# Optimization experiments

Measured on AMD Instinct MI355X. Metric: run time of the kernel, lower is better.

The kernel has to match this reference:

```python
import jax, jax.numpy as jnp
import numpy as np

N, K, D, L = 4096, 64, 1024, 16384  # tokens, top-k, d_in, num_latents


def setup_inputs() -> dict:
    key = jax.random.key(0)
    ks = jax.random.split(key, 9)
    x = jax.random.normal(ks[0], (N, D), jnp.float32)
    y = jax.random.normal(ks[1], (N, D), jnp.float32)
    latent_acts = jax.random.uniform(ks[2], (N, K), jnp.float32)  # post-topk acts (nonneg)
    latent_indices = jax.random.randint(ks[3], (N, K), 0, L)
    W_dec = jax.random.normal(ks[4], (L, D), jnp.float32) / np.sqrt(D).astype(np.float32)
    b_dec = jax.random.normal(ks[5], (D,), jnp.float32) * 0.01
    post_enc = jax.random.normal(ks[6], (L,), jnp.float32) * 0.01
    post_enc_scale = 1.0 + 0.1 * jax.random.normal(ks[7], (L,), jnp.float32)
    W_skip = jax.random.normal(ks[8], (D, D), jnp.float32) / np.sqrt(D).astype(np.float32)
    return {
        "x": x, "y": y,
        "latent_acts": latent_acts, "latent_indices": latent_indices,
        "W_dec": W_dec, "b_dec": b_dec,
        "post_enc": post_enc, "post_enc_scale": post_enc_scale,
        "W_skip": W_skip,
    }


def reference(x, y, latent_acts, latent_indices, W_dec, b_dec, post_enc, post_enc_scale, W_skip):
    # current_latent_acts: per-index bias gather + indexed scaling
    acts = (latent_acts + post_enc[latent_indices]) * post_enc_scale[latent_indices]  # [N,K]
    # decode: gather W_dec rows by top-k indices, weighted combine, add decoder bias
    sae_out = jnp.einsum('nk,nkd->nd', acts, W_dec[latent_indices]) + b_dec  # [N,D]
    # skip connection: x @ W_skip.mT
    sae_out = sae_out + x @ W_skip.T
    # FVU loss
    e = y - sae_out
    total_variance = jnp.sum((y - jnp.mean(y, axis=0)) ** 2)
    fvu = jnp.sum(e ** 2) / total_variance
    return sae_out, fvu
```

## Files before the change

### kernel.cpp

```cpp
#include <hip/hip_runtime.h>
#include <hip/hip_bf16.h>
#include <cstdint>

#define N_TOK 4096
#define KTOP  64
#define DIM   1024
#define NLAT  16384
#define NCHUNK 8

typedef __bf16 bf16x8 __attribute__((ext_vector_type(8)));
typedef float  floatx4 __attribute__((ext_vector_type(4)));
typedef float  floatx2 __attribute__((ext_vector_type(2)));

#define GLOBAL_AS(p) ((const __attribute__((address_space(1))) void*)(p))
#define LDS_AS(p)    ((__attribute__((address_space(3))) void*)(p))

__device__ inline unsigned short f2bf(float f){
  unsigned int u = __float_as_uint(f);
  unsigned int r = (u + 0x7fffu + ((u >> 16) & 1u)) >> 16;
  return (unsigned short)r;
}

__global__ __launch_bounds__(256) void prep(
    const float* __restrict__ x, const float* __restrict__ Wsk,
    const float* __restrict__ Wd, const float* __restrict__ y,
    unsigned short* __restrict__ xb, unsigned short* __restrict__ wb,
    unsigned char* __restrict__ wdf,
    float* __restrict__ colsum, float* __restrict__ sumsq){
  const int b = blockIdx.x;
  const int t = threadIdx.x;
  if (b < 1024){
    int i0 = b * 1024 + t;
    #pragma unroll
    for (int i = 0; i < 4; i++){
      float4 v = ((const float4*)x)[i0 + i * 256];
      ushort4 o; o.x = f2bf(v.x); o.y = f2bf(v.y); o.z = f2bf(v.z); o.w = f2bf(v.w);
      ((ushort4*)xb)[i0 + i * 256] = o;
    }
  } else if (b < 1280){
    int i0 = (b - 1024) * 1024 + t;
    #pragma unroll
    for (int i = 0; i < 4; i++){
      float4 v = ((const float4*)Wsk)[i0 + i * 256];
      ushort4 o; o.x = f2bf(v.x); o.y = f2bf(v.y); o.z = f2bf(v.z); o.w = f2bf(v.w);
      ((ushort4*)wb)[i0 + i * 256] = o;
    }
  } else if (b < 3328){
    int lat0 = (b - 1280) * 8;
    const int chunk = t >> 5;
    const int off   = (t & 31) * 4;
    #pragma unroll
    for (int r = 0; r < 8; r++){
      int lat = lat0 + r;
      float4 v = ((const float4*)(Wd + (size_t)lat * DIM))[t];
      int p = __builtin_amdgcn_cvt_pk_fp8_f32(v.x, v.y, 0, false);
      p     = __builtin_amdgcn_cvt_pk_fp8_f32(v.z, v.w, p, true);
      *(int*)(wdf + ((size_t)chunk * NLAT + lat) * 128 + off) = p;
    }
  } else {
    const int r0 = (b - 3328) * 8;
    float4 cs = {0.f, 0.f, 0.f, 0.f};
    float sq = 0.f;
    #pragma unroll
    for (int r = 0; r < 8; r++){
      float4 v = ((const float4*)(y + (size_t)(r0 + r) * DIM))[t];
      cs.x += v.x; cs.y += v.y; cs.z += v.z; cs.w += v.w;
      sq += v.x*v.x + v.y*v.y + v.z*v.z + v.w*v.w;
    }
    atomicAdd(&colsum[t*4+0], cs.x);
    atomicAdd(&colsum[t*4+1], cs.y);
    atomicAdd(&colsum[t*4+2], cs.z);
    atomicAdd(&colsum[t*4+3], cs.w);
    #pragma unroll
    for (int off = 32; off > 0; off >>= 1) sq += __shfl_down(sq, off, 64);
    __shared__ float s_red[4];
    if ((t & 63) == 0) s_red[t >> 6] = sq;
    __syncthreads();
    if (t == 0) atomicAdd(sumsq, s_red[0] + s_red[1] + s_red[2] + s_red[3]);
  }
}

__global__ __launch_bounds__(256) void skip_gemm(
    const unsigned short* __restrict__ xb,
    const unsigned short* __restrict__ wb,
    const float* __restrict__ b_dec,
    float* __restrict__ out){
  __shared__ unsigned short As[128][32];
  __shared__ unsigned short Bs[64][32];
  const int row0 = blockIdx.x * 128;
  const int col0 = blockIdx.y * 64;
  const int t    = threadIdx.x;
  const int lane = t & 63;
  const int w    = t >> 6;
  const int wr   = w * 32;
  const int lm   = lane & 15;
  const int kq   = lane >> 4;
  const int sr   = t >> 2;
  const int sc   = (t & 3) * 8;

  floatx4 acc[2][4] = {};

  for (int k0 = 0; k0 < DIM; k0 += 32){
    __builtin_amdgcn_global_load_lds(GLOBAL_AS(xb + (size_t)(row0 + sr) * DIM + k0 + sc),
                                     LDS_AS(&As[sr][sc]), 16, 0, 0);
    __builtin_amdgcn_global_load_lds(GLOBAL_AS(xb + (size_t)(row0 + 64 + sr) * DIM + k0 + sc),
                                     LDS_AS(&As[64 + sr][sc]), 16, 0, 0);
    __builtin_amdgcn_global_load_lds(GLOBAL_AS(wb + (size_t)(col0 + sr) * DIM + k0 + sc),
                                     LDS_AS(&Bs[sr][sc]), 16, 0, 0);
    __syncthreads();
    bf16x8 af[2], bfr[4];
    #pragma unroll
    for (int mi = 0; mi < 2; mi++) af[mi] = *(const bf16x8*)(&As[wr + mi * 16 + lm][kq * 8]);
    #pragma unroll
    for (int ni = 0; ni < 4; ni++) bfr[ni] = *(const bf16x8*)(&Bs[ni * 16 + lm][kq * 8]);
    #pragma unroll
    for (int mi = 0; mi < 2; mi++)
      #pragma unroll
      for (int ni = 0; ni < 4; ni++)
        acc[mi][ni] = __builtin_amdgcn_mfma_f32_16x16x32_bf16(af[mi], bfr[ni], acc[mi][ni], 0, 0, 0);
    __syncthreads();
  }

  const int rq = (lane >> 4) * 4;
  #pragma unroll
  for (int mi = 0; mi < 2; mi++){
    #pragma unroll
    for (int ni = 0; ni < 4; ni++){
      int col = col0 + ni * 16 + lm;
      float bd = b_dec[col];
      #pragma unroll
      for (int r = 0; r < 4; r++){
        int row = row0 + wr + mi * 16 + rq + r;
        out[(size_t)row * DIM + col] = acc[mi][ni][r] + bd;
      }
    }
  }
}

__global__ __launch_bounds__(256) void decode_residual(
    const float* __restrict__ y,
    const float* __restrict__ la,
    const int*   __restrict__ li,
    const unsigned char* __restrict__ Wdf,
    const float* __restrict__ pe,
    const float* __restrict__ pes,
    float* __restrict__ out,
    float* __restrict__ sse){
  const int chunk = blockIdx.x & 7;
  const int tok0  = (blockIdx.x >> 3) * 16;
  const int t  = threadIdx.x;
  const int tl = t >> 4;
  const int cl = t & 15;
  __shared__ uint2 s_ai[16][66];
  __shared__ float s_red[4];
  #pragma unroll
  for (int i = 0; i < 4; i++){
    int e = t + i * 256;
    int tok = e >> 6, k = e & 63;
    int id = li[(tok0 + tok) * KTOP + k];
    float a = (la[(tok0 + tok) * KTOP + k] + pe[id]) * pes[id];
    s_ai[tok][k] = make_uint2(__float_as_uint(a), (unsigned)id * 128u);
  }
  __syncthreads();
  const int n = tok0 + tl;
  const unsigned char* Wbase = Wdf + (size_t)chunk * NLAT * 128 + cl * 8;
  float* op = out + (size_t)n * DIM + chunk * 128 + cl * 8;
  const float* yp = y + (size_t)n * DIM + chunk * 128 + cl * 8;
  float4 o0 = ((const float4*)op)[0], o1 = ((const float4*)op)[1];
  float4 y0 = ((const float4*)yp)[0], y1 = ((const float4*)yp)[1];
  float acc[8] = {};
  #pragma unroll 16
  for (int k = 0; k < KTOP; k++){
    uint2 p = s_ai[tl][k];
    const float a = __uint_as_float(p.x);
    const uint2 wv = *(const uint2*)(Wbase + p.y);
    floatx2 c0 = __builtin_amdgcn_cvt_pk_f32_fp8(wv.x, false);
    floatx2 c1 = __builtin_amdgcn_cvt_pk_f32_fp8(wv.x, true);
    floatx2 c2 = __builtin_amdgcn_cvt_pk_f32_fp8(wv.y, false);
    floatx2 c3 = __builtin_amdgcn_cvt_pk_f32_fp8(wv.y, true);
    acc[0] += a * c0.x; acc[1] += a * c0.y;
    acc[2] += a * c1.x; acc[3] += a * c1.y;
    acc[4] += a * c2.x; acc[5] += a * c2.y;
    acc[6] += a * c3.x; acc[7] += a * c3.y;
  }
  acc[0] += o0.x; acc[1] += o0.y; acc[2] += o0.z; acc[3] += o0.w;
  acc[4] += o1.x; acc[5] += o1.y; acc[6] += o1.z; acc[7] += o1.w;
  ((float4*)op)[0] = make_float4(acc[0], acc[1], acc[2], acc[3]);
  ((float4*)op)[1] = make_float4(acc[4], acc[5], acc[6], acc[7]);
  float e0 = y0.x - acc[0], e1 = y0.y - acc[1], e2 = y0.z - acc[2], e3 = y0.w - acc[3];
  float e4 = y1.x - acc[4], e5 = y1.y - acc[5], e6 = y1.z - acc[6], e7 = y1.w - acc[7];
  float s = e0*e0 + e1*e1 + e2*e2 + e3*e3 + e4*e4 + e5*e5 + e6*e6 + e7*e7;
  #pragma unroll
  for (int off = 32; off > 0; off >>= 1) s += __shfl_down(s, off, 64);
  if ((t & 63) == 0) s_red[t >> 6] = s;
  __syncthreads();
  if (t == 0) atomicAdd(sse, s_red[0] + s_red[1] + s_red[2] + s_red[3]);
}

__global__ __launch_bounds__(256) void fvu_kernel(
    const float* __restrict__ ws, float* __restrict__ fvu_out){
  const int t = threadIdx.x;
  float4 c = ((const float4*)(ws + 4))[t];
  float s = c.x*c.x + c.y*c.y + c.z*c.z + c.w*c.w;
  #pragma unroll
  for (int off = 32; off > 0; off >>= 1) s += __shfl_down(s, off, 64);
  __shared__ float s_red[4];
  if ((t & 63) == 0) s_red[t >> 6] = s;
  __syncthreads();
  if (t == 0){
    float ss = s_red[0] + s_red[1] + s_red[2] + s_red[3];
    float tv = ws[1] - ss / (float)N_TOK;
    fvu_out[0] = ws[0] / tv;
  }
}

extern "C" void kernel_launch(void* const* d_in, const int* in_sizes, int n_in,
                              void* d_out, int out_size, void* d_ws, size_t ws_size,
                              hipStream_t stream){
  const float* x   = (const float*)d_in[0];
  const float* y   = (const float*)d_in[1];
  const float* la  = (const float*)d_in[2];
  const int*   li  = (const int*)d_in[3];
  const float* Wd  = (const float*)d_in[4];
  const float* bd  = (const float*)d_in[5];
  const float* pe  = (const float*)d_in[6];
  const float* pes = (const float*)d_in[7];
  const float* Wsk = (const float*)d_in[8];
  float* out = (float*)d_out;

  float* accs = (float*)d_ws;
  unsigned short* xb  = (unsigned short*)((char*)d_ws + 8192);
  unsigned short* wb  = xb + (size_t)N_TOK * DIM;
  unsigned char*  wdf = (unsigned char*)(wb + (size_t)DIM * DIM);

  hipMemsetAsync(d_ws, 0, 8192, stream);
  prep<<<3840, 256, 0, stream>>>(x, Wsk, Wd, y, xb, wb, wdf, accs + 4, accs + 1);
  skip_gemm<<<dim3(N_TOK / 128, DIM / 64), 256, 0, stream>>>(xb, wb, bd, out);
  decode_residual<<<(N_TOK / 16) * NCHUNK, 256, 0, stream>>>(y, la, li, wdf, pe, pes, out, accs);
  fvu_kernel<<<1, 256, 0, stream>>>(accs, out + (size_t)N_TOK * DIM);
}
```

Measured before the change: 266.5 us.

## Load fp32 x directly into skip GEMM and drop separate bf16 conversion pass

The prep kernel no longer converts x to bf16. The skip GEMM now loads fp32 x tiles into LDS with an XOR-swizzled layout and truncates them to bf16 in registers with byte permutes before the MFMA. This removes a full write and reread of the bf16 copy of x, but doubles the A-tile LDS footprint and global read volume inside the GEMM, and it truncates instead of rounding to nearest. The y-statistics blocks are also coarsened to 32 rows per block to cut the number of atomics.

```diff
diff --git a/kernel.cpp b/kernel.cpp
--- a/kernel.cpp
+++ b/kernel.cpp
@@ -22,31 +22,34 @@
 }
 
 __global__ __launch_bounds__(256) void prep(
-    const float* __restrict__ x, const float* __restrict__ Wsk,
-    const float* __restrict__ Wd, const float* __restrict__ y,
-    unsigned short* __restrict__ xb, unsigned short* __restrict__ wb,
-    unsigned char* __restrict__ wdf,
+    const float* __restrict__ Wsk, const float* __restrict__ Wd,
+    const float* __restrict__ y,
+    unsigned short* __restrict__ wb, unsigned char* __restrict__ wdf,
     float* __restrict__ colsum, float* __restrict__ sumsq){
   const int b = blockIdx.x;
   const int t = threadIdx.x;
-  if (b < 1024){
-    int i0 = b * 1024 + t;
-    #pragma unroll
-    for (int i = 0; i < 4; i++){
-      float4 v = ((const float4*)x)[i0 + i * 256];
-      ushort4 o; o.x = f2bf(v.x); o.y = f2bf(v.y); o.z = f2bf(v.z); o.w = f2bf(v.w);
-      ((ushort4*)xb)[i0 + i * 256] = o;
-    }
-  } else if (b < 1280){
-    int i0 = (b - 1024) * 1024 + t;
-    #pragma unroll
-    for (int i = 0; i < 4; i++){
-      float4 v = ((const float4*)Wsk)[i0 + i * 256];
-      ushort4 o; o.x = f2bf(v.x); o.y = f2bf(v.y); o.z = f2bf(v.z); o.w = f2bf(v.w);
-      ((ushort4*)wb)[i0 + i * 256] = o;
-    }
-  } else if (b < 3328){
-    int lat0 = (b - 1280) * 8;
+  if (b < 128){
+    const int r0 = b * 32;
+    float4 cs = {0.f, 0.f, 0.f, 0.f};
+    float sq = 0.f;
+    #pragma unroll 4
+    for (int r = 0; r < 32; r++){
+      float4 v = ((const float4*)(y + (size_t)(r0 + r) * DIM))[t];
+      cs.x += v.x; cs.y += v.y; cs.z += v.z; cs.w += v.w;
+      sq += v.x*v.x + v.y*v.y + v.z*v.z + v.w*v.w;
+    }
+    atomicAdd(&colsum[t*4+0], cs.x);
+    atomicAdd(&colsum[t*4+1], cs.y);
+    atomicAdd(&colsum[t*4+2], cs.z);
+    atomicAdd(&colsum[t*4+3], cs.w);
+    #pragma unroll
+    for (int off = 32; off > 0; off >>= 1) sq += __shfl_down(sq, off, 64);
+    __shared__ float s_red[4];
+    if ((t & 63) == 0) s_red[t >> 6] = sq;
+    __syncthreads();
+    if (t == 0) atomicAdd(sumsq, s_red[0] + s_red[1] + s_red[2] + s_red[3]);
+  } else if (b < 2176){
+    int lat0 = (b - 128) * 8;
     const int chunk = t >> 5;
     const int off   = (t & 31) * 4;
     #pragma unroll
@@ -58,34 +61,22 @@
       *(int*)(wdf + ((size_t)chunk * NLAT + lat) * 128 + off) = p;
     }
   } else {
-    const int r0 = (b - 3328) * 8;
-    float4 cs = {0.f, 0.f, 0.f, 0.f};
-    float sq = 0.f;
-    #pragma unroll
-    for (int r = 0; r < 8; r++){
-      float4 v = ((const float4*)(y + (size_t)(r0 + r) * DIM))[t];
-      cs.x += v.x; cs.y += v.y; cs.z += v.z; cs.w += v.w;
-      sq += v.x*v.x + v.y*v.y + v.z*v.z + v.w*v.w;
-    }
-    atomicAdd(&colsum[t*4+0], cs.x);
-    atomicAdd(&colsum[t*4+1], cs.y);
-    atomicAdd(&colsum[t*4+2], cs.z);
-    atomicAdd(&colsum[t*4+3], cs.w);
-    #pragma unroll
-    for (int off = 32; off > 0; off >>= 1) sq += __shfl_down(sq, off, 64);
-    __shared__ float s_red[4];
-    if ((t & 63) == 0) s_red[t >> 6] = sq;
-    __syncthreads();
-    if (t == 0) atomicAdd(sumsq, s_red[0] + s_red[1] + s_red[2] + s_red[3]);
+    int i0 = (b - 2176) * 1024 + t;
+    #pragma unroll
+    for (int i = 0; i < 4; i++){
+      float4 v = ((const float4*)Wsk)[i0 + i * 256];
+      ushort4 o; o.x = f2bf(v.x); o.y = f2bf(v.y); o.z = f2bf(v.z); o.w = f2bf(v.w);
+      ((ushort4*)wb)[i0 + i * 256] = o;
+    }
   }
 }
 
 __global__ __launch_bounds__(256) void skip_gemm(
-    const unsigned short* __restrict__ xb,
+    const float* __restrict__ x,
     const unsigned short* __restrict__ wb,
     const float* __restrict__ b_dec,
     float* __restrict__ out){
-  __shared__ unsigned short As[128][32];
+  __shared__ float As[128][32];
   __shared__ unsigned short Bs[64][32];
   const int row0 = blockIdx.x * 128;
   const int col0 = blockIdx.y * 64;
@@ -95,22 +86,38 @@
   const int wr   = w * 32;
   const int lm   = lane & 15;
   const int kq   = lane >> 4;
-  const int sr   = t >> 2;
-  const int sc   = (t & 3) * 8;
+  const int ar = t >> 3;
+  const int ag = (t & 7) ^ (ar & 7);
+  const int brow = t >> 2;
+  const int bcol = (t & 3) * 8;
 
   floatx4 acc[2][4] = {};
 
   for (int k0 = 0; k0 < DIM; k0 += 32){
-    __builtin_amdgcn_global_load_lds(GLOBAL_AS(xb + (size_t)(row0 + sr) * DIM + k0 + sc),
-                                     LDS_AS(&As[sr][sc]), 16, 0, 0);
-    __builtin_amdgcn_global_load_lds(GLOBAL_AS(xb + (size_t)(row0 + 64 + sr) * DIM + k0 + sc),
-                                     LDS_AS(&As[64 + sr][sc]), 16, 0, 0);
-    __builtin_amdgcn_global_load_lds(GLOBAL_AS(wb + (size_t)(col0 + sr) * DIM + k0 + sc),
-                                     LDS_AS(&Bs[sr][sc]), 16, 0, 0);
+    #pragma unroll
+    for (int i = 0; i < 4; i++){
+      __builtin_amdgcn_global_load_lds(
+          GLOBAL_AS(x + (size_t)(row0 + i * 32 + ar) * DIM + k0 + ag * 4),
+          LDS_AS(&As[i * 32 + ar][(t & 7) * 4]), 16, 0, 0);
+    }
+    __builtin_amdgcn_global_load_lds(GLOBAL_AS(wb + (size_t)(col0 + brow) * DIM + k0 + bcol),
+                                     LDS_AS(&Bs[brow][bcol]), 16, 0, 0);
     __syncthreads();
     bf16x8 af[2], bfr[4];
     #pragma unroll
-    for (int mi = 0; mi < 2; mi++) af[mi] = *(const bf16x8*)(&As[wr + mi * 16 + lm][kq * 8]);
+    for (int mi = 0; mi < 2; mi++){
+      const int r = wr + mi * 16 + lm;
+      const int c0 = (2 * kq) ^ (r & 7);
+      const int c1 = (2 * kq + 1) ^ (r & 7);
+      float4 f0 = *(const float4*)(&As[r][c0 * 4]);
+      float4 f1 = *(const float4*)(&As[r][c1 * 4]);
+      union { bf16x8 v; unsigned int u[4]; } pk;
+      pk.u[0] = __builtin_amdgcn_perm(__float_as_uint(f0.y), __float_as_uint(f0.x), 0x07060302);
+      pk.u[1] = __builtin_amdgcn_perm(__float_as_uint(f0.w), __float_as_uint(f0.z), 0x07060302);
+      pk.u[2] = __builtin_amdgcn_perm(__float_as_uint(f1.y), __float_as_uint(f1.x), 0x07060302);
+      pk.u[3] = __builtin_amdgcn_perm(__float_as_uint(f1.w), __float_as_uint(f1.z), 0x07060302);
+      af[mi] = pk.v;
+    }
     #pragma unroll
     for (int ni = 0; ni < 4; ni++) bfr[ni] = *(const bf16x8*)(&Bs[ni * 16 + lm][kq * 8]);
     #pragma unroll
@@ -229,13 +236,12 @@
   float* out = (float*)d_out;
 
   float* accs = (float*)d_ws;
-  unsigned short* xb  = (unsigned short*)((char*)d_ws + 8192);
-  unsigned short* wb  = xb + (size_t)N_TOK * DIM;
+  unsigned short* wb  = (unsigned short*)((char*)d_ws + 8192);
   unsigned char*  wdf = (unsigned char*)(wb + (size_t)DIM * DIM);
 
   hipMemsetAsync(d_ws, 0, 8192, stream);
-  prep<<<3840, 256, 0, stream>>>(x, Wsk, Wd, y, xb, wb, wdf, accs + 4, accs + 1);
-  skip_gemm<<<dim3(N_TOK / 128, DIM / 64), 256, 0, stream>>>(xb, wb, bd, out);
+  prep<<<2432, 256, 0, stream>>>(Wsk, Wd, y, wb, wdf, accs + 4, accs + 1);
+  skip_gemm<<<dim3(N_TOK / 128, DIM / 64), 256, 0, stream>>>(x, wb, bd, out);
   decode_residual<<<(N_TOK / 16) * NCHUNK, 256, 0, stream>>>(y, la, li, wdf, pe, pes, out, accs);
   fvu_kernel<<<1, 256, 0, stream>>>(accs, out + (size_t)N_TOK * DIM);
 }
```

New measurement: 229.6 us. -13.9%, faster.

## Fuse prep, skip GEMM, decode and FVU into one persistent kernel with grid barriers

Applied to the files above, without the earlier changes.

Replaces the four kernel launches with a single persistent kernel of 512 blocks that walks the prep, GEMM, decode-residual and FVU phases, separating them with software grid barriers. Column-sum and sum-of-squares atomics give way to per-block partial buffers that are reduced deterministically after a barrier. The aim is to remove launch gaps and atomic contention. In exchange, each phase is limited to 512 blocks, which lowers parallelism for the decode phase, and correctness depends on all blocks being co-resident.

```diff
diff --git a/kernel.cpp b/kernel.cpp
--- a/kernel.cpp
+++ b/kernel.cpp
@@ -6,7 +6,7 @@
 #define KTOP  64
 #define DIM   1024
 #define NLAT  16384
-#define NCHUNK 8
+#define NBLK  512
 
 typedef __bf16 bf16x8 __attribute__((ext_vector_type(8)));
 typedef float  floatx4 __attribute__((ext_vector_type(4)));
@@ -17,200 +17,253 @@
 
 __device__ inline unsigned short f2bf(float f){
   unsigned int u = __float_as_uint(f);
-  unsigned int r = (u + 0x7fffu + ((u >> 16) & 1u)) >> 16;
-  return (unsigned short)r;
-}
-
-__global__ __launch_bounds__(256) void prep(
-    const float* __restrict__ x, const float* __restrict__ Wsk,
-    const float* __restrict__ Wd, const float* __restrict__ y,
+  return (unsigned short)((u + 0x7fffu + ((u >> 16) & 1u)) >> 16);
+}
+
+__device__ inline void gridbar(unsigned* cnt, unsigned* gen){
+  __threadfence();
+  __syncthreads();
+  if (threadIdx.x == 0){
+    unsigned g = __hip_atomic_load(gen, __ATOMIC_RELAXED, __HIP_MEMORY_SCOPE_AGENT);
+    unsigned a = __hip_atomic_fetch_add(cnt, 1u, __ATOMIC_ACQ_REL, __HIP_MEMORY_SCOPE_AGENT);
+    if (a == NBLK - 1){
+      __hip_atomic_store(cnt, 0u, __ATOMIC_RELAXED, __HIP_MEMORY_SCOPE_AGENT);
+      __hip_atomic_store(gen, g + 1u, __ATOMIC_RELEASE, __HIP_MEMORY_SCOPE_AGENT);
+    } else {
+      while (__hip_atomic_load(gen, __ATOMIC_ACQUIRE, __HIP_MEMORY_SCOPE_AGENT) == g)
+        __builtin_amdgcn_s_sleep(8);
+    }
+  }
+  __syncthreads();
+  __threadfence();
+}
+
+__global__ __launch_bounds__(256, 2) void fused(
+    const float* __restrict__ x,  const float* __restrict__ y,
+    const float* __restrict__ la, const int* __restrict__ li,
+    const float* __restrict__ Wd, const float* __restrict__ bd,
+    const float* __restrict__ pe, const float* __restrict__ pes,
+    const float* __restrict__ Wsk, float* __restrict__ out,
+    unsigned* __restrict__ bar,
     unsigned short* __restrict__ xb, unsigned short* __restrict__ wb,
     unsigned char* __restrict__ wdf,
-    float* __restrict__ colsum, float* __restrict__ sumsq){
-  const int b = blockIdx.x;
-  const int t = threadIdx.x;
-  if (b < 1024){
-    int i0 = b * 1024 + t;
-    #pragma unroll
-    for (int i = 0; i < 4; i++){
-      float4 v = ((const float4*)x)[i0 + i * 256];
-      ushort4 o; o.x = f2bf(v.x); o.y = f2bf(v.y); o.z = f2bf(v.z); o.w = f2bf(v.w);
-      ((ushort4*)xb)[i0 + i * 256] = o;
-    }
-  } else if (b < 1280){
-    int i0 = (b - 1024) * 1024 + t;
-    #pragma unroll
-    for (int i = 0; i < 4; i++){
-      float4 v = ((const float4*)Wsk)[i0 + i * 256];
-      ushort4 o; o.x = f2bf(v.x); o.y = f2bf(v.y); o.z = f2bf(v.z); o.w = f2bf(v.w);
-      ((ushort4*)wb)[i0 + i * 256] = o;
-    }
-  } else if (b < 3328){
-    int lat0 = (b - 1280) * 8;
-    const int chunk = t >> 5;
-    const int off   = (t & 31) * 4;
-    #pragma unroll
-    for (int r = 0; r < 8; r++){
-      int lat = lat0 + r;
-      float4 v = ((const float4*)(Wd + (size_t)lat * DIM))[t];
-      int p = __builtin_amdgcn_cvt_pk_fp8_f32(v.x, v.y, 0, false);
-      p     = __builtin_amdgcn_cvt_pk_fp8_f32(v.z, v.w, p, true);
-      *(int*)(wdf + ((size_t)chunk * NLAT + lat) * 128 + off) = p;
-    }
-  } else {
-    const int r0 = (b - 3328) * 8;
-    float4 cs = {0.f, 0.f, 0.f, 0.f};
-    float sq = 0.f;
-    #pragma unroll
-    for (int r = 0; r < 8; r++){
-      float4 v = ((const float4*)(y + (size_t)(r0 + r) * DIM))[t];
-      cs.x += v.x; cs.y += v.y; cs.z += v.z; cs.w += v.w;
-      sq += v.x*v.x + v.y*v.y + v.z*v.z + v.w*v.w;
-    }
-    atomicAdd(&colsum[t*4+0], cs.x);
-    atomicAdd(&colsum[t*4+1], cs.y);
-    atomicAdd(&colsum[t*4+2], cs.z);
-    atomicAdd(&colsum[t*4+3], cs.w);
-    #pragma unroll
-    for (int off = 32; off > 0; off >>= 1) sq += __shfl_down(sq, off, 64);
-    __shared__ float s_red[4];
-    if ((t & 63) == 0) s_red[t >> 6] = sq;
-    __syncthreads();
-    if (t == 0) atomicAdd(sumsq, s_red[0] + s_red[1] + s_red[2] + s_red[3]);
-  }
-}
-
-__global__ __launch_bounds__(256) void skip_gemm(
-    const unsigned short* __restrict__ xb,
-    const unsigned short* __restrict__ wb,
-    const float* __restrict__ b_dec,
-    float* __restrict__ out){
-  __shared__ unsigned short As[128][32];
-  __shared__ unsigned short Bs[64][32];
-  const int row0 = blockIdx.x * 128;
-  const int col0 = blockIdx.y * 64;
-  const int t    = threadIdx.x;
-  const int lane = t & 63;
-  const int w    = t >> 6;
-  const int wr   = w * 32;
-  const int lm   = lane & 15;
-  const int kq   = lane >> 4;
-  const int sr   = t >> 2;
-  const int sc   = (t & 3) * 8;
-
-  floatx4 acc[2][4] = {};
-
-  for (int k0 = 0; k0 < DIM; k0 += 32){
-    __builtin_amdgcn_global_load_lds(GLOBAL_AS(xb + (size_t)(row0 + sr) * DIM + k0 + sc),
-                                     LDS_AS(&As[sr][sc]), 16, 0, 0);
-    __builtin_amdgcn_global_load_lds(GLOBAL_AS(xb + (size_t)(row0 + 64 + sr) * DIM + k0 + sc),
-                                     LDS_AS(&As[64 + sr][sc]), 16, 0, 0);
-    __builtin_amdgcn_global_load_lds(GLOBAL_AS(wb + (size_t)(col0 + sr) * DIM + k0 + sc),
-                                     LDS_AS(&Bs[sr][sc]), 16, 0, 0);
-    __syncthreads();
-    bf16x8 af[2], bfr[4];
-    #pragma unroll
-    for (int mi = 0; mi < 2; mi++) af[mi] = *(const bf16x8*)(&As[wr + mi * 16 + lm][kq * 8]);
-    #pragma unroll
-    for (int ni = 0; ni < 4; ni++) bfr[ni] = *(const bf16x8*)(&Bs[ni * 16 + lm][kq * 8]);
-    #pragma unroll
-    for (int mi = 0; mi < 2; mi++)
-      #pragma unroll
-      for (int ni = 0; ni < 4; ni++)
-        acc[mi][ni] = __builtin_amdgcn_mfma_f32_16x16x32_bf16(af[mi], bfr[ni], acc[mi][ni], 0, 0, 0);
-    __syncthreads();
-  }
-
-  const int rq = (lane >> 4) * 4;
-  #pragma unroll
-  for (int mi = 0; mi < 2; mi++){
-    #pragma unroll
-    for (int ni = 0; ni < 4; ni++){
-      int col = col0 + ni * 16 + lm;
-      float bd = b_dec[col];
-      #pragma unroll
-      for (int r = 0; r < 4; r++){
-        int row = row0 + wr + mi * 16 + rq + r;
-        out[(size_t)row * DIM + col] = acc[mi][ni][r] + bd;
-      }
-    }
-  }
-}
-
-__global__ __launch_bounds__(256) void decode_residual(
-    const float* __restrict__ y,
-    const float* __restrict__ la,
-    const int*   __restrict__ li,
-    const unsigned char* __restrict__ Wdf,
-    const float* __restrict__ pe,
-    const float* __restrict__ pes,
-    float* __restrict__ out,
-    float* __restrict__ sse){
-  const int chunk = blockIdx.x & 7;
-  const int tok0  = (blockIdx.x >> 3) * 16;
-  const int t  = threadIdx.x;
-  const int tl = t >> 4;
-  const int cl = t & 15;
-  __shared__ uint2 s_ai[16][66];
-  __shared__ float s_red[4];
-  #pragma unroll
-  for (int i = 0; i < 4; i++){
-    int e = t + i * 256;
-    int tok = e >> 6, k = e & 63;
-    int id = li[(tok0 + tok) * KTOP + k];
-    float a = (la[(tok0 + tok) * KTOP + k] + pe[id]) * pes[id];
-    s_ai[tok][k] = make_uint2(__float_as_uint(a), (unsigned)id * 128u);
+    float* __restrict__ csp,
+    float* __restrict__ ssep,
+    float* __restrict__ sqp,
+    float* __restrict__ vp,
+    float* __restrict__ sqf)
+{
+  __shared__ __align__(16) char smem[12352];
+  const int bid = blockIdx.x;
+  const int t   = threadIdx.x;
+
+  for (int u = bid; u < 3456; u += NBLK){
+    if (u < 1024){
+      int i0 = u * 1024 + t;
+      #pragma unroll
+      for (int i = 0; i < 4; i++){
+        float4 v = ((const float4*)x)[i0 + i * 256];
+        ushort4 o; o.x = f2bf(v.x); o.y = f2bf(v.y); o.z = f2bf(v.z); o.w = f2bf(v.w);
+        ((ushort4*)xb)[i0 + i * 256] = o;
+      }
+    } else if (u < 1280){
+      int i0 = (u - 1024) * 1024 + t;
+      #pragma unroll
+      for (int i = 0; i < 4; i++){
+        float4 v = ((const float4*)Wsk)[i0 + i * 256];
+        ushort4 o; o.x = f2bf(v.x); o.y = f2bf(v.y); o.z = f2bf(v.z); o.w = f2bf(v.w);
+        ((ushort4*)wb)[i0 + i * 256] = o;
+      }
+    } else if (u < 3328){
+      int lat0 = (u - 1280) * 8;
+      const int chunk = t >> 5;
+      const int off   = (t & 31) * 4;
+      #pragma unroll
+      for (int r = 0; r < 8; r++){
+        int lat = lat0 + r;
+        float4 v = ((const float4*)(Wd + (size_t)lat * DIM))[t];
+        int p = __builtin_amdgcn_cvt_pk_fp8_f32(v.x, v.y, 0, false);
+        p     = __builtin_amdgcn_cvt_pk_fp8_f32(v.z, v.w, p, true);
+        *(int*)(wdf + ((size_t)chunk * NLAT + lat) * 128 + off) = p;
+      }
+    } else {
+      int p = u - 3328;
+      const int r0 = p * 32;
+      float4 cs = {0.f, 0.f, 0.f, 0.f};
+      float sq = 0.f;
+      #pragma unroll 4
+      for (int r = 0; r < 32; r++){
+        float4 v = ((const float4*)(y + (size_t)(r0 + r) * DIM))[t];
+        cs.x += v.x; cs.y += v.y; cs.z += v.z; cs.w += v.w;
+        sq += v.x*v.x + v.y*v.y + v.z*v.z + v.w*v.w;
+      }
+      ((float4*)(csp + (size_t)p * 1024))[t] = cs;
+      #pragma unroll
+      for (int off = 32; off > 0; off >>= 1) sq += __shfl_down(sq, off, 64);
+      float* sred = (float*)smem;
+      __syncthreads();
+      if ((t & 63) == 0) sred[t >> 6] = sq;
+      __syncthreads();
+      if (t == 0) sqp[p] = sred[0] + sred[1] + sred[2] + sred[3];
+      __syncthreads();
+    }
+  }
+  gridbar(bar, bar + 1);
+
+  if (bid < 32){
+    float* red = (float*)smem;
+    const int c  = bid * 32 + (t & 31);
+    const int pg = t >> 5;
+    float s = 0.f;
+    for (int p = pg; p < 128; p += 8) s += csp[(size_t)p * 1024 + c];
+    red[pg * 32 + (t & 31)] = s;
+    __syncthreads();
+    float cs = 0.f;
+    if (t < 32){
+      #pragma unroll
+      for (int g = 0; g < 8; g++) cs += red[g * 32 + t];
+    }
+    float v = cs * cs;
+    #pragma unroll
+    for (int off = 16; off > 0; off >>= 1) v += __shfl_down(v, off, 64);
+    if (t == 0) vp[bid] = v;
+  } else if (bid == 32){
+    float v2 = (t < 128) ? sqp[t] : 0.f;
+    #pragma unroll
+    for (int off = 32; off > 0; off >>= 1) v2 += __shfl_down(v2, off, 64);
+    float* red2 = (float*)smem;
+    if ((t & 63) == 0) red2[t >> 6] = v2;
+    __syncthreads();
+    if (t == 0) sqf[0] = red2[0] + red2[1] + red2[2] + red2[3];
   }
   __syncthreads();
-  const int n = tok0 + tl;
-  const unsigned char* Wbase = Wdf + (size_t)chunk * NLAT * 128 + cl * 8;
-  float* op = out + (size_t)n * DIM + chunk * 128 + cl * 8;
-  const float* yp = y + (size_t)n * DIM + chunk * 128 + cl * 8;
-  float4 o0 = ((const float4*)op)[0], o1 = ((const float4*)op)[1];
-  float4 y0 = ((const float4*)yp)[0], y1 = ((const float4*)yp)[1];
-  float acc[8] = {};
-  #pragma unroll 16
-  for (int k = 0; k < KTOP; k++){
-    uint2 p = s_ai[tl][k];
-    const float a = __uint_as_float(p.x);
-    const uint2 wv = *(const uint2*)(Wbase + p.y);
-    floatx2 c0 = __builtin_amdgcn_cvt_pk_f32_fp8(wv.x, false);
-    floatx2 c1 = __builtin_amdgcn_cvt_pk_f32_fp8(wv.x, true);
-    floatx2 c2 = __builtin_amdgcn_cvt_pk_f32_fp8(wv.y, false);
-    floatx2 c3 = __builtin_amdgcn_cvt_pk_f32_fp8(wv.y, true);
-    acc[0] += a * c0.x; acc[1] += a * c0.y;
-    acc[2] += a * c1.x; acc[3] += a * c1.y;
-    acc[4] += a * c2.x; acc[5] += a * c2.y;
-    acc[6] += a * c3.x; acc[7] += a * c3.y;
-  }
-  acc[0] += o0.x; acc[1] += o0.y; acc[2] += o0.z; acc[3] += o0.w;
-  acc[4] += o1.x; acc[5] += o1.y; acc[6] += o1.z; acc[7] += o1.w;
-  ((float4*)op)[0] = make_float4(acc[0], acc[1], acc[2], acc[3]);
-  ((float4*)op)[1] = make_float4(acc[4], acc[5], acc[6], acc[7]);
-  float e0 = y0.x - acc[0], e1 = y0.y - acc[1], e2 = y0.z - acc[2], e3 = y0.w - acc[3];
-  float e4 = y1.x - acc[4], e5 = y1.y - acc[5], e6 = y1.z - acc[6], e7 = y1.w - acc[7];
-  float s = e0*e0 + e1*e1 + e2*e2 + e3*e3 + e4*e4 + e5*e5 + e6*e6 + e7*e7;
-  #pragma unroll
-  for (int off = 32; off > 0; off >>= 1) s += __shfl_down(s, off, 64);
-  if ((t & 63) == 0) s_red[t >> 6] = s;
-  __syncthreads();
-  if (t == 0) atomicAdd(sse, s_red[0] + s_red[1] + s_red[2] + s_red[3]);
-}
-
-__global__ __launch_bounds__(256) void fvu_kernel(
-    const float* __restrict__ ws, float* __restrict__ fvu_out){
-  const int t = threadIdx.x;
-  float4 c = ((const float4*)(ws + 4))[t];
-  float s = c.x*c.x + c.y*c.y + c.z*c.z + c.w*c.w;
-  #pragma unroll
-  for (int off = 32; off > 0; off >>= 1) s += __shfl_down(s, off, 64);
-  __shared__ float s_red[4];
-  if ((t & 63) == 0) s_red[t >> 6] = s;
-  __syncthreads();
-  if (t == 0){
-    float ss = s_red[0] + s_red[1] + s_red[2] + s_red[3];
-    float tv = ws[1] - ss / (float)N_TOK;
-    fvu_out[0] = ws[0] / tv;
+
+  {
+    unsigned short (*As)[32] = (unsigned short(*)[32])smem;
+    unsigned short (*Bs)[32] = (unsigned short(*)[32])(smem + 8192);
+    const int row0 = (bid >> 4) * 128;
+    const int col0 = (bid & 15) * 64;
+    const int lane = t & 63;
+    const int w    = t >> 6;
+    const int wr   = w * 32;
+    const int lm   = lane & 15;
+    const int kq   = lane >> 4;
+    const int sr   = t >> 2;
+    const int sc   = (t & 3) * 8;
+
+    floatx4 acc[2][4] = {};
+
+    for (int k0 = 0; k0 < DIM; k0 += 32){
+      __builtin_amdgcn_global_load_lds(GLOBAL_AS(xb + (size_t)(row0 + sr) * DIM + k0 + sc),
+                                       LDS_AS(&As[sr][sc]), 16, 0, 0);
+      __builtin_amdgcn_global_load_lds(GLOBAL_AS(xb + (size_t)(row0 + 64 + sr) * DIM + k0 + sc),
+                                       LDS_AS(&As[64 + sr][sc]), 16, 0, 0);
+      __builtin_amdgcn_global_load_lds(GLOBAL_AS(wb + (size_t)(col0 + sr) * DIM + k0 + sc),
+                                       LDS_AS(&Bs[sr][sc]), 16, 0, 0);
+      __syncthreads();
+      bf16x8 af[2], bfr[4];
+      #pragma unroll
+      for (int mi = 0; mi < 2; mi++) af[mi] = *(const bf16x8*)(&As[wr + mi * 16 + lm][kq * 8]);
+      #pragma unroll
+      for (int ni = 0; ni < 4; ni++) bfr[ni] = *(const bf16x8*)(&Bs[ni * 16 + lm][kq * 8]);
+      #pragma unroll
+      for (int mi = 0; mi < 2; mi++)
+        #pragma unroll
+        for (int ni = 0; ni < 4; ni++)
+          acc[mi][ni] = __builtin_amdgcn_mfma_f32_16x16x32_bf16(af[mi], bfr[ni], acc[mi][ni], 0, 0, 0);
+      __syncthreads();
+    }
+
+    const int rq = (lane >> 4) * 4;
+    #pragma unroll
+    for (int mi = 0; mi < 2; mi++){
+      #pragma unroll
+      for (int ni = 0; ni < 4; ni++){
+        int col = col0 + ni * 16 + lm;
+        float bdv = bd[col];
+        #pragma unroll
+        for (int r = 0; r < 4; r++){
+          int row = row0 + wr + mi * 16 + rq + r;
+          out[(size_t)row * DIM + col] = acc[mi][ni][r] + bdv;
+        }
+      }
+    }
+  }
+  gridbar(bar, bar + 1);
+
+  {
+    uint2 (*s_ai)[66] = (uint2(*)[66])smem;
+    float* sred = (float*)(smem + 12288);
+    const int tl = t >> 4;
+    const int cl = t & 15;
+    float sacc = 0.f;
+    #pragma unroll
+    for (int it = 0; it < 4; it++){
+      const int vb    = bid + it * NBLK;
+      const int chunk = vb & 7;
+      const int tok0  = (vb >> 3) * 16;
+      __syncthreads();
+      #pragma unroll
+      for (int i = 0; i < 4; i++){
+        int e = t + i * 256;
+        int tok = e >> 6, k = e & 63;
+        int id = li[(tok0 + tok) * KTOP + k];
+        float a = (la[(tok0 + tok) * KTOP + k] + pe[id]) * pes[id];
+        s_ai[tok][k] = make_uint2(__float_as_uint(a), (unsigned)id * 128u);
+      }
+      __syncthreads();
+      const int n = tok0 + tl;
+      const unsigned char* Wbase = wdf + (size_t)chunk * NLAT * 128 + cl * 8;
+      float* op = out + (size_t)n * DIM + chunk * 128 + cl * 8;
+      const float* yp = y + (size_t)n * DIM + chunk * 128 + cl * 8;
+      float4 o0 = ((const float4*)op)[0], o1 = ((const float4*)op)[1];
+      float4 y0 = ((const float4*)yp)[0], y1 = ((const float4*)yp)[1];
+      float acc[8] = {};
+      #pragma unroll 16
+      for (int k = 0; k < KTOP; k++){
+        uint2 p = s_ai[tl][k];
+        const float a = __uint_as_float(p.x);
+        const uint2 wv = *(const uint2*)(Wbase + p.y);
+        floatx2 c0 = __builtin_amdgcn_cvt_pk_f32_fp8(wv.x, false);
+        floatx2 c1 = __builtin_amdgcn_cvt_pk_f32_fp8(wv.x, true);
+        floatx2 c2 = __builtin_amdgcn_cvt_pk_f32_fp8(wv.y, false);
+        floatx2 c3 = __builtin_amdgcn_cvt_pk_f32_fp8(wv.y, true);
+        acc[0] += a * c0.x; acc[1] += a * c0.y;
+        acc[2] += a * c1.x; acc[3] += a * c1.y;
+        acc[4] += a * c2.x; acc[5] += a * c2.y;
+        acc[6] += a * c3.x; acc[7] += a * c3.y;
+      }
+      acc[0] += o0.x; acc[1] += o0.y; acc[2] += o0.z; acc[3] += o0.w;
+      acc[4] += o1.x; acc[5] += o1.y; acc[6] += o1.z; acc[7] += o1.w;
+      ((float4*)op)[0] = make_float4(acc[0], acc[1], acc[2], acc[3]);
+      ((float4*)op)[1] = make_float4(acc[4], acc[5], acc[6], acc[7]);
+      float e0 = y0.x - acc[0], e1 = y0.y - acc[1], e2 = y0.z - acc[2], e3 = y0.w - acc[3];
+      float e4 = y1.x - acc[4], e5 = y1.y - acc[5], e6 = y1.z - acc[6], e7 = y1.w - acc[7];
+      sacc += e0*e0 + e1*e1 + e2*e2 + e3*e3 + e4*e4 + e5*e5 + e6*e6 + e7*e7;
+    }
+    #pragma unroll
+    for (int off = 32; off > 0; off >>= 1) sacc += __shfl_down(sacc, off, 64);
+    if ((t & 63) == 0) sred[t >> 6] = sacc;
+    __syncthreads();
+    if (t == 0) ssep[bid] = sred[0] + sred[1] + sred[2] + sred[3];
+  }
+  gridbar(bar, bar + 1);
+
+  if (bid == 0){
+    float s = ssep[t] + ssep[t + 256];
+    #pragma unroll
+    for (int off = 32; off > 0; off >>= 1) s += __shfl_down(s, off, 64);
+    float* sred = (float*)smem;
+    __syncthreads();
+    if ((t & 63) == 0) sred[t >> 6] = s;
+    __syncthreads();
+    if (t == 0){
+      float sse = sred[0] + sred[1] + sred[2] + sred[3];
+      float var = 0.f;
+      for (int i = 0; i < 32; i++) var += vp[i];
+      float tv = sqf[0] - var / (float)N_TOK;
+      out[(size_t)N_TOK * DIM] = sse / tv;
+    }
   }
 }
 
@@ -228,14 +281,18 @@
   const float* Wsk = (const float*)d_in[8];
   float* out = (float*)d_out;
 
-  float* accs = (float*)d_ws;
-  unsigned short* xb  = (unsigned short*)((char*)d_ws + 8192);
-  unsigned short* wb  = xb + (size_t)N_TOK * DIM;
-  unsigned char*  wdf = (unsigned char*)(wb + (size_t)DIM * DIM);
-
-  hipMemsetAsync(d_ws, 0, 8192, stream);
-  prep<<<3840, 256, 0, stream>>>(x, Wsk, Wd, y, xb, wb, wdf, accs + 4, accs + 1);
-  skip_gemm<<<dim3(N_TOK / 128, DIM / 64), 256, 0, stream>>>(xb, wb, bd, out);
-  decode_residual<<<(N_TOK / 16) * NCHUNK, 256, 0, stream>>>(y, la, li, wdf, pe, pes, out, accs);
-  fvu_kernel<<<1, 256, 0, stream>>>(accs, out + (size_t)N_TOK * DIM);
-}
+  char* w = (char*)d_ws;
+  unsigned* bar = (unsigned*)w;
+  unsigned short* xb  = (unsigned short*)(w + 4096);
+  unsigned short* wb  = (unsigned short*)(w + 4096 + (8u << 20));
+  unsigned char*  wdf = (unsigned char*)(w + 4096 + (10u << 20));
+  float* csp  = (float*)(w + 4096 + (26u << 20));
+  float* ssep = (float*)(w + 4096 + (26u << 20) + (512u << 10));
+  float* sqp  = ssep + 512;
+  float* vp   = sqp + 128;
+  float* sqf  = vp + 32;
+
+  hipMemsetAsync(bar, 0, 64, stream);
+  fused<<<NBLK, 256, 0, stream>>>(x, y, la, li, Wd, bd, pe, pes, Wsk, out,
+                                  bar, xb, wb, wdf, csp, ssep, sqp, vp, sqf);
+}
```

After: 759.8 us. +185.1%, slower.

## Replace atomics and memset with partial-sum buffers and last-block FVU reduction

Applied to the files above, without the earlier changes.

Removes the hipMemsetAsync and the separate fvu kernel. Column sums and sum-of-squares of y become per-block partials that skip_gemm blocks reduce, and decode_residual finishes the FVU in a last-block-done pattern. The decode kernel now handles 32 tokens per block with 16 columns per thread using 128-bit fp8 loads, and prep block counts are rebalanced. This cuts launches and contended float atomics, at the cost of extra work in the GEMM prologue and an extra barrier there.

```diff
diff --git a/kernel.cpp b/kernel.cpp
--- a/kernel.cpp
+++ b/kernel.cpp
@@ -6,7 +6,6 @@
 #define KTOP  64
 #define DIM   1024
 #define NLAT  16384
-#define NCHUNK 8
 
 typedef __bf16 bf16x8 __attribute__((ext_vector_type(8)));
 typedef float  floatx4 __attribute__((ext_vector_type(4)));
@@ -17,8 +16,7 @@
 
 __device__ inline unsigned short f2bf(float f){
   unsigned int u = __float_as_uint(f);
-  unsigned int r = (u + 0x7fffu + ((u >> 16) & 1u)) >> 16;
-  return (unsigned short)r;
+  return (unsigned short)((u + 0x7fffu + ((u >> 16) & 1u)) >> 16);
 }
 
 __global__ __launch_bounds__(256) void prep(
@@ -26,57 +24,56 @@
     const float* __restrict__ Wd, const float* __restrict__ y,
     unsigned short* __restrict__ xb, unsigned short* __restrict__ wb,
     unsigned char* __restrict__ wdf,
-    float* __restrict__ colsum, float* __restrict__ sumsq){
+    float* __restrict__ csp, float* __restrict__ sqp,
+    unsigned* __restrict__ done){
   const int b = blockIdx.x;
   const int t = threadIdx.x;
-  if (b < 1024){
-    int i0 = b * 1024 + t;
+  if (b == 0 && t == 0) *done = 0u;
+  if (b < 256){
+    const int r0 = b * 16;
+    float4 cs = {0.f, 0.f, 0.f, 0.f};
+    float sq = 0.f;
+    #pragma unroll 4
+    for (int r = 0; r < 16; r++){
+      float4 v = ((const float4*)(y + (size_t)(r0 + r) * DIM))[t];
+      cs.x += v.x; cs.y += v.y; cs.z += v.z; cs.w += v.w;
+      sq += v.x*v.x + v.y*v.y + v.z*v.z + v.w*v.w;
+    }
+    ((float4*)(csp + (size_t)b * DIM))[t] = cs;
+    #pragma unroll
+    for (int off = 32; off > 0; off >>= 1) sq += __shfl_down(sq, off, 64);
+    __shared__ float sred[4];
+    if ((t & 63) == 0) sred[t >> 6] = sq;
+    __syncthreads();
+    if (t == 0) sqp[b] = sred[0] + sred[1] + sred[2] + sred[3];
+  } else if (b < 1280){
+    int i0 = (b - 256) * 1024 + t;
     #pragma unroll
     for (int i = 0; i < 4; i++){
       float4 v = ((const float4*)x)[i0 + i * 256];
       ushort4 o; o.x = f2bf(v.x); o.y = f2bf(v.y); o.z = f2bf(v.z); o.w = f2bf(v.w);
       ((ushort4*)xb)[i0 + i * 256] = o;
     }
-  } else if (b < 1280){
-    int i0 = (b - 1024) * 1024 + t;
+  } else if (b < 1536){
+    int i0 = (b - 1280) * 1024 + t;
     #pragma unroll
     for (int i = 0; i < 4; i++){
       float4 v = ((const float4*)Wsk)[i0 + i * 256];
       ushort4 o; o.x = f2bf(v.x); o.y = f2bf(v.y); o.z = f2bf(v.z); o.w = f2bf(v.w);
       ((ushort4*)wb)[i0 + i * 256] = o;
     }
-  } else if (b < 3328){
-    int lat0 = (b - 1280) * 8;
+  } else {
+    int lat0 = (b - 1536) * 4;
     const int chunk = t >> 5;
     const int off   = (t & 31) * 4;
     #pragma unroll
-    for (int r = 0; r < 8; r++){
+    for (int r = 0; r < 4; r++){
       int lat = lat0 + r;
       float4 v = ((const float4*)(Wd + (size_t)lat * DIM))[t];
       int p = __builtin_amdgcn_cvt_pk_fp8_f32(v.x, v.y, 0, false);
       p     = __builtin_amdgcn_cvt_pk_fp8_f32(v.z, v.w, p, true);
       *(int*)(wdf + ((size_t)chunk * NLAT + lat) * 128 + off) = p;
     }
-  } else {
-    const int r0 = (b - 3328) * 8;
-    float4 cs = {0.f, 0.f, 0.f, 0.f};
-    float sq = 0.f;
-    #pragma unroll
-    for (int r = 0; r < 8; r++){
-      float4 v = ((const float4*)(y + (size_t)(r0 + r) * DIM))[t];
-      cs.x += v.x; cs.y += v.y; cs.z += v.z; cs.w += v.w;
-      sq += v.x*v.x + v.y*v.y + v.z*v.z + v.w*v.w;
-    }
-    atomicAdd(&colsum[t*4+0], cs.x);
-    atomicAdd(&colsum[t*4+1], cs.y);
-    atomicAdd(&colsum[t*4+2], cs.z);
-    atomicAdd(&colsum[t*4+3], cs.w);
-    #pragma unroll
-    for (int off = 32; off > 0; off >>= 1) sq += __shfl_down(sq, off, 64);
-    __shared__ float s_red[4];
-    if ((t & 63) == 0) s_red[t >> 6] = sq;
-    __syncthreads();
-    if (t == 0) atomicAdd(sumsq, s_red[0] + s_red[1] + s_red[2] + s_red[3]);
   }
 }
 
@@ -84,12 +81,39 @@
     const unsigned short* __restrict__ xb,
     const unsigned short* __restrict__ wb,
     const float* __restrict__ b_dec,
+    const float* __restrict__ csp, const float* __restrict__ sqp,
+    float* __restrict__ vp, float* __restrict__ sqf,
     float* __restrict__ out){
   __shared__ unsigned short As[128][32];
   __shared__ unsigned short Bs[64][32];
+  __shared__ float sred[4];
+  const int bid = blockIdx.y * 32 + blockIdx.x;
+  const int t   = threadIdx.x;
+
+  if (bid < 256){
+    const int g    = t >> 6;
+    const int lane = t & 63;
+    const int col  = bid * 4 + g;
+    float s = 0.f;
+    #pragma unroll
+    for (int j = 0; j < 4; j++) s += csp[(size_t)(lane + 64 * j) * DIM + col];
+    #pragma unroll
+    for (int off = 32; off > 0; off >>= 1) s += __shfl_down(s, off, 64);
+    if (lane == 0) sred[g] = s * s;
+    __syncthreads();
+    if (t == 0) vp[bid] = sred[0] + sred[1] + sred[2] + sred[3];
+  } else if (bid == 256){
+    float v = sqp[t];
+    #pragma unroll
+    for (int off = 32; off > 0; off >>= 1) v += __shfl_down(v, off, 64);
+    if ((t & 63) == 0) sred[t >> 6] = v;
+    __syncthreads();
+    if (t == 0) sqf[0] = sred[0] + sred[1] + sred[2] + sred[3];
+  }
+  __syncthreads();
+
   const int row0 = blockIdx.x * 128;
   const int col0 = blockIdx.y * 64;
-  const int t    = threadIdx.x;
   const int lane = t & 63;
   const int w    = t >> 6;
   const int wr   = w * 32;
@@ -127,11 +151,11 @@
     #pragma unroll
     for (int ni = 0; ni < 4; ni++){
       int col = col0 + ni * 16 + lm;
-      float bd = b_dec[col];
+      float bdv = b_dec[col];
       #pragma unroll
       for (int r = 0; r < 4; r++){
         int row = row0 + wr + mi * 16 + rq + r;
-        out[(size_t)row * DIM + col] = acc[mi][ni][r] + bd;
+        out[(size_t)row * DIM + col] = acc[mi][ni][r] + bdv;
       }
     }
   }
@@ -141,20 +165,24 @@
     const float* __restrict__ y,
     const float* __restrict__ la,
     const int*   __restrict__ li,
-    const unsigned char* __restrict__ Wdf,
+    const unsigned char* __restrict__ wdf,
     const float* __restrict__ pe,
     const float* __restrict__ pes,
     float* __restrict__ out,
-    float* __restrict__ sse){
-  const int chunk = blockIdx.x & 7;
-  const int tok0  = (blockIdx.x >> 3) * 16;
+    float* __restrict__ ssep,
+    const float* __restrict__ vp, const float* __restrict__ sqf,
+    unsigned* __restrict__ done){
+  const int bid   = blockIdx.x;
+  const int chunk = bid & 7;
+  const int tok0  = (bid >> 3) * 32;
   const int t  = threadIdx.x;
-  const int tl = t >> 4;
-  const int cl = t & 15;
-  __shared__ uint2 s_ai[16][66];
-  __shared__ float s_red[4];
-  #pragma unroll
-  for (int i = 0; i < 4; i++){
+  const int tl = t >> 3;
+  const int cl = t & 7;
+  __shared__ uint2 s_ai[32][65];
+  __shared__ float sred[4], sred2[4];
+  __shared__ int lastflag;
+  #pragma unroll
+  for (int i = 0; i < 8; i++){
     int e = t + i * 256;
     int tok = e >> 6, k = e & 63;
     int id = li[(tok0 + tok) * KTOP + k];
@@ -163,54 +191,63 @@
   }
   __syncthreads();
   const int n = tok0 + tl;
-  const unsigned char* Wbase = Wdf + (size_t)chunk * NLAT * 128 + cl * 8;
-  float* op = out + (size_t)n * DIM + chunk * 128 + cl * 8;
-  const float* yp = y + (size_t)n * DIM + chunk * 128 + cl * 8;
-  float4 o0 = ((const float4*)op)[0], o1 = ((const float4*)op)[1];
-  float4 y0 = ((const float4*)yp)[0], y1 = ((const float4*)yp)[1];
-  float acc[8] = {};
-  #pragma unroll 16
+  const unsigned char* Wbase = wdf + (size_t)chunk * NLAT * 128 + cl * 16;
+  float* op = out + (size_t)n * DIM + chunk * 128 + cl * 16;
+  const float* yp = y + (size_t)n * DIM + chunk * 128 + cl * 16;
+  float acc[16] = {};
+  #pragma unroll 8
   for (int k = 0; k < KTOP; k++){
     uint2 p = s_ai[tl][k];
     const float a = __uint_as_float(p.x);
-    const uint2 wv = *(const uint2*)(Wbase + p.y);
-    floatx2 c0 = __builtin_amdgcn_cvt_pk_f32_fp8(wv.x, false);
-    floatx2 c1 = __builtin_amdgcn_cvt_pk_f32_fp8(wv.x, true);
-    floatx2 c2 = __builtin_amdgcn_cvt_pk_f32_fp8(wv.y, false);
-    floatx2 c3 = __builtin_amdgcn_cvt_pk_f32_fp8(wv.y, true);
-    acc[0] += a * c0.x; acc[1] += a * c0.y;
-    acc[2] += a * c1.x; acc[3] += a * c1.y;
-    acc[4] += a * c2.x; acc[5] += a * c2.y;
-    acc[6] += a * c3.x; acc[7] += a * c3.y;
-  }
-  acc[0] += o0.x; acc[1] += o0.y; acc[2] += o0.z; acc[3] += o0.w;
-  acc[4] += o1.x; acc[5] += o1.y; acc[6] += o1.z; acc[7] += o1.w;
-  ((float4*)op)[0] = make_float4(acc[0], acc[1], acc[2], acc[3]);
-  ((float4*)op)[1] = make_float4(acc[4], acc[5], acc[6], acc[7]);
-  float e0 = y0.x - acc[0], e1 = y0.y - acc[1], e2 = y0.z - acc[2], e3 = y0.w - acc[3];
-  float e4 = y1.x - acc[4], e5 = y1.y - acc[5], e6 = y1.z - acc[6], e7 = y1.w - acc[7];
-  float s = e0*e0 + e1*e1 + e2*e2 + e3*e3 + e4*e4 + e5*e5 + e6*e6 + e7*e7;
+    const uint4 wv = *(const uint4*)(Wbase + p.y);
+    floatx2 c;
+    c = __builtin_amdgcn_cvt_pk_f32_fp8(wv.x, false); acc[0]  += a*c.x; acc[1]  += a*c.y;
+    c = __builtin_amdgcn_cvt_pk_f32_fp8(wv.x, true ); acc[2]  += a*c.x; acc[3]  += a*c.y;
+    c = __builtin_amdgcn_cvt_pk_f32_fp8(wv.y, false); acc[4]  += a*c.x; acc[5]  += a*c.y;
+    c = __builtin_amdgcn_cvt_pk_f32_fp8(wv.y, true ); acc[6]  += a*c.x; acc[7]  += a*c.y;
+    c = __builtin_amdgcn_cvt_pk_f32_fp8(wv.z, false); acc[8]  += a*c.x; acc[9]  += a*c.y;
+    c = __builtin_amdgcn_cvt_pk_f32_fp8(wv.z, true ); acc[10] += a*c.x; acc[11] += a*c.y;
+    c = __builtin_amdgcn_cvt_pk_f32_fp8(wv.w, false); acc[12] += a*c.x; acc[13] += a*c.y;
+    c = __builtin_amdgcn_cvt_pk_f32_fp8(wv.w, true ); acc[14] += a*c.x; acc[15] += a*c.y;
+  }
+  float s = 0.f;
+  #pragma unroll
+  for (int q = 0; q < 4; q++){
+    float4 o  = ((const float4*)op)[q];
+    float4 yv = ((const float4*)yp)[q];
+    float4 r;
+    r.x = acc[4*q+0] + o.x; r.y = acc[4*q+1] + o.y;
+    r.z = acc[4*q+2] + o.z; r.w = acc[4*q+3] + o.w;
+    ((float4*)op)[q] = r;
+    float e0 = yv.x - r.x, e1 = yv.y - r.y, e2 = yv.z - r.z, e3 = yv.w - r.w;
+    s += e0*e0 + e1*e1 + e2*e2 + e3*e3;
+  }
   #pragma unroll
   for (int off = 32; off > 0; off >>= 1) s += __shfl_down(s, off, 64);
-  if ((t & 63) == 0) s_red[t >> 6] = s;
-  __syncthreads();
-  if (t == 0) atomicAdd(sse, s_red[0] + s_red[1] + s_red[2] + s_red[3]);
-}
-
-__global__ __launch_bounds__(256) void fvu_kernel(
-    const float* __restrict__ ws, float* __restrict__ fvu_out){
-  const int t = threadIdx.x;
-  float4 c = ((const float4*)(ws + 4))[t];
-  float s = c.x*c.x + c.y*c.y + c.z*c.z + c.w*c.w;
-  #pragma unroll
-  for (int off = 32; off > 0; off >>= 1) s += __shfl_down(s, off, 64);
-  __shared__ float s_red[4];
-  if ((t & 63) == 0) s_red[t >> 6] = s;
+  if ((t & 63) == 0) sred[t >> 6] = s;
   __syncthreads();
   if (t == 0){
-    float ss = s_red[0] + s_red[1] + s_red[2] + s_red[3];
-    float tv = ws[1] - ss / (float)N_TOK;
-    fvu_out[0] = ws[0] / tv;
+    ssep[bid] = sred[0] + sred[1] + sred[2] + sred[3];
+    unsigned old = __hip_atomic_fetch_add(done, 1u, __ATOMIC_ACQ_REL, __HIP_MEMORY_SCOPE_AGENT);
+    lastflag = (old == 1023u);
+  }
+  __syncthreads();
+  if (lastflag){
+    float v = ssep[t] + ssep[t + 256] + ssep[t + 512] + ssep[t + 768];
+    float w = vp[t];
+    #pragma unroll
+    for (int off = 32; off > 0; off >>= 1){
+      v += __shfl_down(v, off, 64);
+      w += __shfl_down(w, off, 64);
+    }
+    if ((t & 63) == 0){ sred[t >> 6] = v; sred2[t >> 6] = w; }
+    __syncthreads();
+    if (t == 0){
+      float sse = sred[0] + sred[1] + sred[2] + sred[3];
+      float var = sred2[0] + sred2[1] + sred2[2] + sred2[3];
+      float tv  = sqf[0] - var / (float)N_TOK;
+      out[(size_t)N_TOK * DIM] = sse / tv;
+    }
   }
 }
 
@@ -228,14 +265,18 @@
   const float* Wsk = (const float*)d_in[8];
   float* out = (float*)d_out;
 
-  float* accs = (float*)d_ws;
-  unsigned short* xb  = (unsigned short*)((char*)d_ws + 8192);
-  unsigned short* wb  = xb + (size_t)N_TOK * DIM;
-  unsigned char*  wdf = (unsigned char*)(wb + (size_t)DIM * DIM);
-
-  hipMemsetAsync(d_ws, 0, 8192, stream);
-  prep<<<3840, 256, 0, stream>>>(x, Wsk, Wd, y, xb, wb, wdf, accs + 4, accs + 1);
-  skip_gemm<<<dim3(N_TOK / 128, DIM / 64), 256, 0, stream>>>(xb, wb, bd, out);
-  decode_residual<<<(N_TOK / 16) * NCHUNK, 256, 0, stream>>>(y, la, li, wdf, pe, pes, out, accs);
-  fvu_kernel<<<1, 256, 0, stream>>>(accs, out + (size_t)N_TOK * DIM);
-}
+  char* w = (char*)d_ws;
+  unsigned short* xb  = (unsigned short*)(w);
+  unsigned short* wb  = (unsigned short*)(w + (8u << 20));
+  unsigned char*  wdf = (unsigned char*)(w + (10u << 20));
+  float* csp  = (float*)(w + (26u << 20));
+  float* sqp  = (float*)(w + (27u << 20));
+  float* vp   = (float*)(w + (27u << 20) + 4096);
+  float* sqf  = (float*)(w + (27u << 20) + 8192);
+  float* ssep = (float*)(w + (27u << 20) + 12288);
+  unsigned* done = (unsigned*)(w + (27u << 20) + 28672);
+
+  prep<<<5632, 256, 0, stream>>>(x, Wsk, Wd, y, xb, wb, wdf, csp, sqp, done);
+  skip_gemm<<<dim3(32, 16), 256, 0, stream>>>(xb, wb, bd, csp, sqp, vp, sqf, out);
+  decode_residual<<<1024, 256, 0, stream>>>(y, la, li, wdf, pe, pes, out, ssep, vp, sqf, done);
+}
```

Measured after the change: 241.9 us. 1.1x faster.
